# Kernel tuning notes

Hardware: AMD Instinct MI355X
Metric: run time of the kernel (lower is better)

## Reference

```python
import jax, jax.numpy as jnp
import numpy as np


def setup_inputs() -> dict:
    key = jax.random.key(0)
    k1, k2 = jax.random.split(key)
    N, K, D = 32768, 8192, 256
    inputs = jax.random.normal(k1, (N, D), dtype=jnp.float32)
    embedding = jax.random.normal(k2, (K, D), dtype=jnp.float32)  # codebook buffer
    return {"inputs": inputs, "embedding": embedding}


def reference(inputs, embedding):
    # distances[n, k] = ||x_n||^2 + ||e_k||^2 - 2 <x_n, e_k>   (squared L2, as in torch source)
    x_sq = jnp.sum(inputs * inputs, axis=1, keepdims=True)          # [N, 1]
    e_sq = jnp.sum(embedding * embedding, axis=1)                   # [K]
    cross = inputs @ embedding.T                                    # [N, K]
    distances = x_sq + e_sq - 2.0 * cross                           # [N, K]
    encoding_indices = jnp.argmin(distances, axis=1)                # [N] int
    # torch forward returns (None, None, indices); return the tensor output
    return encoding_indices
```

## Files before the change

### kernel.cpp

```cpp
#include <hip/hip_runtime.h>

constexpr int D_DIM   = 256;
constexpr int N_ROWS  = 32768;
constexpr int K_CODES = 8192;
constexpr unsigned TQ = 58;

typedef _Float16 f16x8  __attribute__((ext_vector_type(8)));
typedef __fp16   fp16x2 __attribute__((ext_vector_type(2)));
typedef float    f32x16 __attribute__((ext_vector_type(16)));

#define MFMA32(a, b, c) __builtin_amdgcn_mfma_f32_32x32x16_f16(a, b, c, 0, 0, 0)

__device__ __forceinline__ void cvt_rtn(const float4 a, const float4 b,
                                        uint4& hi, uint4& lo) {
    float f[8] = {a.x, a.y, a.z, a.w, b.x, b.y, b.z, b.w};
    unsigned hb[8], lb[8];
#pragma unroll
    for (int i = 0; i < 8; ++i) {
        _Float16 h = (_Float16)f[i];
        _Float16 l = (_Float16)(f[i] - (float)h);
        hb[i] = __builtin_bit_cast(unsigned short, h);
        lb[i] = __builtin_bit_cast(unsigned short, l);
    }
    hi = make_uint4(hb[0] | (hb[1] << 16), hb[2] | (hb[3] << 16),
                    hb[4] | (hb[5] << 16), hb[6] | (hb[7] << 16));
    lo = make_uint4(lb[0] | (lb[1] << 16), lb[2] | (lb[3] << 16),
                    lb[4] | (lb[5] << 16), lb[6] | (lb[7] << 16));
}

__device__ __forceinline__ void cvt_granule(const float4 a, const float4 b,
                                            uint4& hi, uint4& lo) {
    fp16x2 h0 = __builtin_amdgcn_cvt_pkrtz(a.x, a.y);
    fp16x2 h1 = __builtin_amdgcn_cvt_pkrtz(a.z, a.w);
    fp16x2 h2 = __builtin_amdgcn_cvt_pkrtz(b.x, b.y);
    fp16x2 h3 = __builtin_amdgcn_cvt_pkrtz(b.z, b.w);
    fp16x2 l0 = __builtin_amdgcn_cvt_pkrtz(a.x - (float)h0.x, a.y - (float)h0.y);
    fp16x2 l1 = __builtin_amdgcn_cvt_pkrtz(a.z - (float)h1.x, a.w - (float)h1.y);
    fp16x2 l2 = __builtin_amdgcn_cvt_pkrtz(b.x - (float)h2.x, b.y - (float)h2.y);
    fp16x2 l3 = __builtin_amdgcn_cvt_pkrtz(b.z - (float)h3.x, b.w - (float)h3.y);
    hi = make_uint4(__builtin_bit_cast(unsigned, h0), __builtin_bit_cast(unsigned, h1),
                    __builtin_bit_cast(unsigned, h2), __builtin_bit_cast(unsigned, h3));
    lo = make_uint4(__builtin_bit_cast(unsigned, l0), __builtin_bit_cast(unsigned, l1),
                    __builtin_bit_cast(unsigned, l2), __builtin_bit_cast(unsigned, l3));
}

__device__ __forceinline__ void gl_lds16(const uint4* g, uint4* l) {
    __builtin_amdgcn_global_load_lds(
        (const __attribute__((address_space(1))) void*)g,
        (__attribute__((address_space(3))) void*)l, 16, 0, 0);
}

__global__ __launch_bounds__(256)
void prep_kernel(const float* __restrict__ X, const float* __restrict__ E,
                 uint4* __restrict__ Xh,
                 uint4* __restrict__ Eh, uint4* __restrict__ El,
                 float* __restrict__ esqb, int* __restrict__ cnt) {
    const int tid = threadIdx.x, bid = blockIdx.x;
    if (bid < 1024) {
#pragma unroll 1
        for (int it = 0; it < 4; ++it) {
            const int gid = bid * 1024 + it * 256 + tid;
            const int rb = gid >> 11, rem = gid & 2047;
            const int Lg = rem >> 6, r = rem & 63;
            const float* p = X + (size_t)(rb * 64 + r) * D_DIM + Lg * 8;
            const float4 a = *(const float4*)p, b = *(const float4*)(p + 4);
            uint4 hi, lo; cvt_rtn(a, b, hi, lo);
            Xh[gid] = hi;
        }
    } else if (bid < 1280) {
#pragma unroll 1
        for (int it = 0; it < 4; ++it) {
            const int gid = (bid - 1024) * 1024 + it * 256 + tid;
            const int cb = gid >> 13, rem = gid & 8191;
            const int Lg = rem >> 8, c = rem & 255;
            const float* p = E + (size_t)(cb * 256 + c) * D_DIM + Lg * 8;
            const float4 a = *(const float4*)p, b = *(const float4*)(p + 4);
            uint4 hi, lo; cvt_rtn(a, b, hi, lo);
            Eh[gid] = hi; El[gid] = lo;
        }
    } else {
        if (bid == 1280 && tid == 0) *cnt = 0;
        const int t = (bid - 1280) * 256 + tid;
        const int gw = t >> 6, lane = t & 63;
        const float4 v = ((const float4*)(E + (size_t)gw * D_DIM))[lane];
        float s = v.x * v.x + v.y * v.y + v.z * v.z + v.w * v.w;
#pragma unroll
        for (int off = 32; off; off >>= 1) s += __shfl_down(s, off, 64);
        if (lane == 0) esqb[gw] = s + 1024.0f;
    }
}

__global__ __launch_bounds__(256, 3)
void vq_pass1(const uint4* __restrict__ Xh, const uint4* __restrict__ Eh,
              const float* __restrict__ esqb, uint2* __restrict__ res) {
    __shared__ uint4 sXh[2048];
    __shared__ uint2 slot[4][64];

    const int tid  = threadIdx.x;
    const int lane = tid & 63, wv = tid >> 6;
    const int l31  = lane & 31, lh = lane >> 5;
    const int bid  = blockIdx.x;
    const int bx = bid & 511, strip = bid >> 9;
    const int cs0 = strip * 2048;

    const uint4* Xhb = Xh + bx * 2048;

#pragma unroll
    for (int i = 0; i < 8; ++i)
        gl_lds16(Xhb + i * 256 + tid, &sXh[i * 256 + (wv << 6)]);
    __syncthreads();

    unsigned best[2][16], best2[2][16];
#pragma unroll
    for (int ti = 0; ti < 2; ++ti)
#pragma unroll
        for (int r = 0; r < 16; ++r) { best[ti][r] = 0xFFFFFFFFu; best2[ti][r] = 0xFFFFFFFFu; }

    f32x16 acc[2][2];

#pragma unroll 1
    for (int ct = 0; ct < 8; ++ct) {
        const uint4* __restrict__ Eb =
            Eh + (size_t)(strip * 8 + ct) * 8192 + wv * 64 + l31;

#pragma unroll
        for (int ti = 0; ti < 2; ++ti)
#pragma unroll
            for (int tj = 0; tj < 2; ++tj)
#pragma unroll
                for (int i = 0; i < 16; ++i) acc[ti][tj][i] = 0.0f;

#pragma unroll 4
        for (int k = 0; k < 16; ++k) {
            const int Lg = k * 2 + lh;
            const f16x8 b0 = __builtin_bit_cast(f16x8, Eb[Lg * 256]);
            const f16x8 b1 = __builtin_bit_cast(f16x8, Eb[Lg * 256 + 32]);
            const f16x8 a0 = __builtin_bit_cast(f16x8, sXh[Lg * 64 + l31]);
            const f16x8 a1 = __builtin_bit_cast(f16x8, sXh[Lg * 64 + l31 + 32]);
            acc[0][0] = MFMA32(a0, b0, acc[0][0]);
            acc[0][1] = MFMA32(a0, b1, acc[0][1]);
            acc[1][0] = MFMA32(a1, b0, acc[1][0]);
            acc[1][1] = MFMA32(a1, b1, acc[1][1]);
        }

#pragma unroll
        for (int tj = 0; tj < 2; ++tj) {
            const int code = cs0 + ct * 256 + wv * 64 + tj * 32 + l31;
            const float eb128 = esqb[code] * 128.0f;
#pragma unroll
            for (int ti = 0; ti < 2; ++ti)
#pragma unroll
                for (int r = 0; r < 16; ++r) {
                    const float dq = fmaf(-256.0f, acc[ti][tj][r], eb128);
                    const unsigned q   = (unsigned)dq;
                    const unsigned key = (q << 13) + (unsigned)code;
                    unsigned nb2;
                    asm("v_med3_u32 %0, %1, %2, %3"
                        : "=v"(nb2)
                        : "v"(key), "v"(best[ti][r]), "v"(best2[ti][r]));
                    best2[ti][r] = nb2;
                    best[ti][r]  = key < best[ti][r] ? key : best[ti][r];
                }
        }
    }

#pragma unroll
    for (int ti = 0; ti < 2; ++ti)
#pragma unroll
        for (int r = 0; r < 16; ++r) {
            unsigned b1 = best[ti][r], b2 = best2[ti][r];
#pragma unroll
            for (int m = 16; m >= 1; m >>= 1) {
                const unsigned o1 = (unsigned)__shfl_xor((int)b1, m, 32);
                const unsigned o2 = (unsigned)__shfl_xor((int)b2, m, 32);
                const unsigned t  = b1 > o1 ? b1 : o1;
                b1 = b1 < o1 ? b1 : o1;
                const unsigned m2 = b2 < o2 ? b2 : o2;
                b2 = m2 < t ? m2 : t;
            }
            if (l31 == 0) {
                const int row = ti * 32 + (r & 3) + 8 * (r >> 2) + 4 * lh;
                slot[wv][row] = make_uint2(b1, b2);
            }
        }

    __syncthreads();
    if (tid < 64) {
        const uint2 A = slot[0][tid];
        unsigned b1 = A.x, b2 = A.y;
#pragma unroll
        for (int s = 1; s < 4; ++s) {
            const uint2 B = slot[s][tid];
            const unsigned t  = b1 > B.x ? b1 : B.x;
            b1 = b1 < B.x ? b1 : B.x;
            const unsigned m2 = b2 < B.y ? b2 : B.y;
            b2 = m2 < t ? m2 : t;
        }
        res[(size_t)strip * N_ROWS + bx * 64 + tid] = make_uint2(b1, b2);
    }
}

__global__ void merge_kernel(const uint2* __restrict__ res,
                             unsigned long long* __restrict__ res0,
                             int* __restrict__ out,
                             int* __restrict__ cnt, int* __restrict__ list) {
    const int row = blockIdx.x * 256 + threadIdx.x;
    unsigned b1 = 0xFFFFFFFFu, b2 = 0xFFFFFFFFu;
#pragma unroll
    for (int s = 0; s < 4; ++s) {
        const uint2 v = res[(size_t)s * N_ROWS + row];
        const unsigned t = b1 > v.x ? b1 : v.x;
        b1 = b1 < v.x ? b1 : v.x;
        const unsigned m2 = b2 < v.y ? b2 : v.y;
        b2 = m2 < t ? m2 : t;
    }
    out[row] = (int)(b1 & 8191u);
    if ((b2 >> 13) - (b1 >> 13) < TQ) {
        const int p = atomicAdd(cnt, 1);
        list[p] = row;
        res0[row] = ~0ull;
    }
}

__global__ __launch_bounds__(256, 1)
void refine_kernel(const float* __restrict__ X,
                   const uint4* __restrict__ Eh, const uint4* __restrict__ El,
                   const float* __restrict__ esqb, const int* __restrict__ cnt,
                   const int* __restrict__ list, unsigned long long* __restrict__ res0) {
    __shared__ int  rows_s[32];
    __shared__ uint4 sAh[1024], sAl[1024];

    const int n = *cnt;
    const int base = blockIdx.x * 32;
    if (base >= n) return;
    const int tid = threadIdx.x;
    if (tid < 32) { const int j = base + tid; rows_s[tid] = list[j < n ? j : base]; }
    __syncthreads();

#pragma unroll
    for (int jj = 0; jj < 4; ++jj) {
        const int gg = jj * 256 + tid, Lg = gg >> 5, rr = gg & 31;
        const int row = rows_s[rr];
        const float* p = X + (size_t)row * D_DIM + Lg * 8;
        const float4 a = *(const float4*)p, b = *(const float4*)(p + 4);
        uint4 hi, lo; cvt_rtn(a, b, hi, lo);
        sAh[Lg * 32 + rr] = hi; sAl[Lg * 32 + rr] = lo;
    }
    __syncthreads();

    const int lane = tid & 63, wv = tid >> 6, l31 = lane & 31, lh = lane >> 5;
    const int cbase = blockIdx.y * 1024 + wv * 256;

    float bestv[16]; int besti[16];
#pragma unroll
    for (int r = 0; r < 16; ++r) { bestv[r] = 3.0e38f; besti[r] = 0; }

#pragma unroll 1
    for (int ps = 0; ps < 2; ++ps) {
        const int c0 = cbase + ps * 128;
        f32x16 acc[4];
#pragma unroll
        for (int tj = 0; tj < 4; ++tj)
#pragma unroll
            for (int i = 0; i < 16; ++i) acc[tj][i] = 0.0f;

#pragma unroll
        for (int ks = 0; ks < 16; ++ks) {
            const int Lg = ks * 2 + lh;
            f16x8 b0[4], b1[4];
#pragma unroll
            for (int tj = 0; tj < 4; ++tj) {
                const int c = c0 + tj * 32 + l31;
                const int eg = (c >> 8) * 8192 + Lg * 256 + (c & 255);
                b0[tj] = __builtin_bit_cast(f16x8, Eh[eg]);
                b1[tj] = __builtin_bit_cast(f16x8, El[eg]);
            }
            const f16x8 a0 = __builtin_bit_cast(f16x8, sAh[Lg * 32 + l31]);
            const f16x8 a1 = __builtin_bit_cast(f16x8, sAl[Lg * 32 + l31]);
#pragma unroll
            for (int tj = 0; tj < 4; ++tj) acc[tj] = MFMA32(a1, b0[tj], acc[tj]);
#pragma unroll
            for (int tj = 0; tj < 4; ++tj) acc[tj] = MFMA32(a0, b1[tj], acc[tj]);
#pragma unroll
            for (int tj = 0; tj < 4; ++tj) acc[tj] = MFMA32(a0, b0[tj], acc[tj]);
        }

#pragma unroll
        for (int tj = 0; tj < 4; ++tj) {
            const int c = c0 + tj * 32 + l31;
            const float eb = esqb[c];
#pragma unroll
            for (int r = 0; r < 16; ++r) {
                const float dv = fmaf(-2.0f, acc[tj][r], eb);
                if (dv < bestv[r]) { bestv[r] = dv; besti[r] = c; }
            }
        }
    }

#pragma unroll
    for (int r = 0; r < 16; ++r) {
        float v = bestv[r]; int bi = besti[r];
#pragma unroll
        for (int m = 16; m >= 1; m >>= 1) {
            const float ov = __shfl_xor(v, m, 32);
            const int   oi = __shfl_xor(bi, m, 32);
            if (ov < v || (ov == v && oi < bi)) { v = ov; bi = oi; }
        }
        if (l31 == 0) {
            const int rl = (r & 3) + 8 * (r >> 2) + 4 * lh;
            atomicMin(&res0[rows_s[rl]],
                      ((unsigned long long)__float_as_uint(v) << 32) | (unsigned)bi);
        }
    }
}

__global__ void finalize_kernel(const unsigned long long* __restrict__ res0,
                                const int* __restrict__ cnt, const int* __restrict__ list,
                                int* __restrict__ out) {
    const int i = blockIdx.x * 256 + threadIdx.x;
    if (i < *cnt) {
        const int row = list[i];
        out[row] = (int)(res0[row] & 0xFFFFFFFFull);
    }
}

__global__ void prologue_fb(const float* __restrict__ E, float* __restrict__ esqb,
                            unsigned long long* __restrict__ packed) {
    const int t = blockIdx.x * 256 + threadIdx.x;
    if (t < N_ROWS) packed[t] = ~0ull;
    const int gw = t >> 6, lane = t & 63;
    const float4 v = ((const float4*)(E + (size_t)gw * D_DIM))[lane];
    float s = v.x * v.x + v.y * v.y + v.z * v.z + v.w * v.w;
#pragma unroll
    for (int off = 32; off; off >>= 1) s += __shfl_down(s, off, 64);
    if (lane == 0) esqb[gw] = s + 1024.0f;
}

__global__ __launch_bounds__(256, 2)
void vq_mfma_fallback(const float* __restrict__ X, const float* __restrict__ E,
                      const float* __restrict__ esqb,
                      unsigned long long* __restrict__ packed) {
    __shared__ uint4 fXh[128 * 8], fXl[128 * 8];
    __shared__ uint4 fEh[128 * 8], fEl[128 * 8];
    __shared__ float fEsq[2048];

    const int tid  = threadIdx.x;
    const int lane = tid & 63;
    const int wv   = tid >> 6;
    const int wr   = wv >> 1, wc = wv & 1;
    const int l31  = lane & 31;
    const int lh   = lane >> 5;
    const int row0 = blockIdx.x * 128;
    const int cs0  = blockIdx.y * 2048;

#pragma unroll
    for (int i = 0; i < 8; ++i) fEsq[tid + 256 * i] = esqb[cs0 + tid + 256 * i];

    const int sr = tid >> 3, sg = tid & 7;

    float best[2][16]; int bidx[2][16];
#pragma unroll
    for (int ti = 0; ti < 2; ++ti)
#pragma unroll
        for (int r = 0; r < 16; ++r) { best[ti][r] = 3.0e38f; bidx[ti][r] = 0; }

    f32x16 acc[2][2];

#pragma unroll 1
    for (int ct = 0; ct < 16; ++ct) {
#pragma unroll
        for (int ti = 0; ti < 2; ++ti)
#pragma unroll
            for (int tj = 0; tj < 2; ++tj)
#pragma unroll
                for (int i = 0; i < 16; ++i) acc[ti][tj][i] = 0.0f;

#pragma unroll 1
        for (int dc = 0; dc < 4; ++dc) {
            __syncthreads();
#pragma unroll
            for (int i = 0; i < 4; ++i) {
                const int r = 32 * i + sr;
                const float* p = X + (size_t)(row0 + r) * D_DIM + dc * 64 + sg * 8;
                const float4 a = *(const float4*)p, b = *(const float4*)(p + 4);
                uint4 hi, lo; cvt_granule(a, b, hi, lo);
                const int o = r * 8 + (sg ^ (r & 7));
                fXh[o] = hi; fXl[o] = lo;
            }
#pragma unroll
            for (int i = 0; i < 4; ++i) {
                const int r = 32 * i + sr;
                const float* p = E + (size_t)(cs0 + ct * 128 + r) * D_DIM + dc * 64 + sg * 8;
                const float4 a = *(const float4*)p, b = *(const float4*)(p + 4);
                uint4 hi, lo; cvt_granule(a, b, hi, lo);
                const int o = r * 8 + (sg ^ (r & 7));
                fEh[o] = hi; fEl[o] = lo;
            }
            __syncthreads();

#pragma unroll
            for (int s = 0; s < 4; ++s) {
                const int gi = s * 2 + lh;
                f16x8 axh[2], axl[2], beh[2], bel[2];
#pragma unroll
                for (int ti = 0; ti < 2; ++ti) {
                    const int r = wr * 64 + ti * 32 + l31;
                    const int o = r * 8 + (gi ^ (r & 7));
                    axh[ti] = __builtin_bit_cast(f16x8, fXh[o]);
                    axl[ti] = __builtin_bit_cast(f16x8, fXl[o]);
                }
#pragma unroll
                for (int tj = 0; tj < 2; ++tj) {
                    const int c = wc * 64 + tj * 32 + l31;
                    const int o = c * 8 + (gi ^ (c & 7));
                    beh[tj] = __builtin_bit_cast(f16x8, fEh[o]);
                    bel[tj] = __builtin_bit_cast(f16x8, fEl[o]);
                }
#pragma unroll
                for (int ti = 0; ti < 2; ++ti)
#pragma unroll
                    for (int tj = 0; tj < 2; ++tj) {
                        acc[ti][tj] = MFMA32(axl[ti], beh[tj], acc[ti][tj]);
                        acc[ti][tj] = MFMA32(axh[ti], bel[tj], acc[ti][tj]);
                        acc[ti][tj] = MFMA32(axh[ti], beh[tj], acc[ti][tj]);
                    }
            }
        }

#pragma unroll
        for (int tj = 0; tj < 2; ++tj) {
            const int cloc = ct * 128 + wc * 64 + tj * 32 + l31;
            const float eb = fEsq[cloc];
            const int  code = cs0 + cloc;
#pragma unroll
            for (int ti = 0; ti < 2; ++ti)
#pragma unroll
                for (int r = 0; r < 16; ++r) {
                    const float dv = fmaf(-2.0f, acc[ti][tj][r], eb);
                    if (dv < best[ti][r]) { best[ti][r] = dv; bidx[ti][r] = code; }
                }
        }
    }

#pragma unroll
    for (int ti = 0; ti < 2; ++ti)
#pragma unroll
        for (int r = 0; r < 16; ++r) {
            float b = best[ti][r]; int bi = bidx[ti][r];
#pragma unroll
            for (int m = 16; m >= 1; m >>= 1) {
                const float ov = __shfl_xor(b, m, 32);
                const int   oi = __shfl_xor(bi, m, 32);
                if (ov < b || (ov == b && oi < bi)) { b = ov; bi = oi; }
            }
            if (l31 == 0) {
                const int row = row0 + wr * 64 + ti * 32 + (r & 3) + 8 * (r >> 2) + 4 * lh;
                const unsigned long long p =
                    ((unsigned long long)__float_as_uint(b) << 32) | (unsigned)bi;
                atomicMin(&packed[row], p);
            }
        }
}

__global__ void finish_fb(const unsigned long long* __restrict__ packed,
                          int* __restrict__ out) {
    const int i = blockIdx.x * 256 + threadIdx.x;
    out[i] = (int)(unsigned)(packed[i] & 0xffffffffull);
}

extern "C" void kernel_launch(void* const* d_in, const int* in_sizes, int n_in,
                              void* d_out, int out_size, void* d_ws, size_t ws_size,
                              hipStream_t stream) {
    const float* X = (const float*)d_in[0];
    const float* E = (const float*)d_in[1];
    char* ws = (char*)d_ws;
    int* out = (int*)d_out;

    float* esqb = (float*)ws;
    uint2* res  = (uint2*)(ws + 32768);
    unsigned long long* res0 = (unsigned long long*)(ws + 1081344);
    int* cnt  = (int*)(ws + 1343488);
    int* list = (int*)(ws + 1343504);
    const size_t base = 1572864;
    const size_t szX  = (size_t)N_ROWS * D_DIM * 2;
    const size_t szE  = (size_t)K_CODES * D_DIM * 2;
    const size_t need = base + szX + 2 * szE;

    if (ws_size >= need) {
        uint4* Xh = (uint4*)(ws + base);
        uint4* Eh = (uint4*)(ws + base + szX);
        uint4* El = (uint4*)(ws + base + szX + szE);
        prep_kernel<<<dim3(3328), dim3(256), 0, stream>>>(X, E, Xh, Eh, El, esqb, cnt);
        vq_pass1<<<dim3(2048), dim3(256), 0, stream>>>(Xh, Eh, esqb, res);
        merge_kernel<<<dim3(N_ROWS / 256), dim3(256), 0, stream>>>(res, res0, out, cnt, list);
        refine_kernel<<<dim3(1024, 8), dim3(256), 0, stream>>>(X, Eh, El, esqb,
                                                               cnt, list, res0);
        finalize_kernel<<<dim3(N_ROWS / 256), dim3(256), 0, stream>>>(res0, cnt, list, out);
    } else {
        unsigned long long* packed = (unsigned long long*)(ws + 32768);
        prologue_fb<<<dim3(2048), dim3(256), 0, stream>>>(E, esqb, packed);
        vq_mfma_fallback<<<dim3(N_ROWS / 128, 4), dim3(256), 0, stream>>>(X, E, esqb, packed);
        finish_fb<<<dim3(N_ROWS / 256), dim3(256), 0, stream>>>(packed, out);
    }
}
```

Before: 327.7 us.

## Software-pipeline codebook fragment loads two steps ahead with MFMA priority boost

Adds register double-buffering of the global codebook fragments in vq_pass1: each K step prefetches the B operands two steps ahead, and the first fragments of the next code tile are loaded before the current tile's argmin epilogue. The inner loop is fully unrolled and the MFMA group is wrapped in s_setprio to favour matrix issue. The occupancy hint drops from 3 to 2 waves per SIMD so the extra live registers fit. This aims to hide global load latency behind MFMA work, at the cost of fewer resident waves to cover other stalls.

```diff
diff --git a/kernel.cpp b/kernel.cpp
--- a/kernel.cpp
+++ b/kernel.cpp
@@ -90,7 +90,7 @@
     }
 }
 
-__global__ __launch_bounds__(256, 3)
+__global__ __launch_bounds__(256, 2)
 void vq_pass1(const uint4* __restrict__ Xh, const uint4* __restrict__ Eh,
               const float* __restrict__ esqb, uint2* __restrict__ res) {
     __shared__ uint4 sXh[2048];
@@ -118,11 +118,15 @@
 
     f32x16 acc[2][2];
 
+    const uint4* __restrict__ Eb = Eh + (size_t)(strip * 8) * 8192 + wv * 64 + l31;
+
+    f16x8 pb0 = __builtin_bit_cast(f16x8, Eb[lh * 256]);
+    f16x8 pb1 = __builtin_bit_cast(f16x8, Eb[lh * 256 + 32]);
+    f16x8 pn0 = __builtin_bit_cast(f16x8, Eb[(2 + lh) * 256]);
+    f16x8 pn1 = __builtin_bit_cast(f16x8, Eb[(2 + lh) * 256 + 32]);
+
 #pragma unroll 1
     for (int ct = 0; ct < 8; ++ct) {
-        const uint4* __restrict__ Eb =
-            Eh + (size_t)(strip * 8 + ct) * 8192 + wv * 64 + l31;
-
 #pragma unroll
         for (int ti = 0; ti < 2; ++ti)
 #pragma unroll
@@ -130,17 +134,35 @@
 #pragma unroll
                 for (int i = 0; i < 16; ++i) acc[ti][tj][i] = 0.0f;
 
-#pragma unroll 4
+        f16x8 c0 = pb0, c1 = pb1;
+        f16x8 n0 = pn0, n1 = pn1;
+
+#pragma unroll
         for (int k = 0; k < 16; ++k) {
             const int Lg = k * 2 + lh;
-            const f16x8 b0 = __builtin_bit_cast(f16x8, Eb[Lg * 256]);
-            const f16x8 b1 = __builtin_bit_cast(f16x8, Eb[Lg * 256 + 32]);
+            f16x8 f0, f1;
+            if (k < 14) {
+                f0 = __builtin_bit_cast(f16x8, Eb[(Lg + 4) * 256]);
+                f1 = __builtin_bit_cast(f16x8, Eb[(Lg + 4) * 256 + 32]);
+            }
             const f16x8 a0 = __builtin_bit_cast(f16x8, sXh[Lg * 64 + l31]);
             const f16x8 a1 = __builtin_bit_cast(f16x8, sXh[Lg * 64 + l31 + 32]);
-            acc[0][0] = MFMA32(a0, b0, acc[0][0]);
-            acc[0][1] = MFMA32(a0, b1, acc[0][1]);
-            acc[1][0] = MFMA32(a1, b0, acc[1][0]);
-            acc[1][1] = MFMA32(a1, b1, acc[1][1]);
+            __builtin_amdgcn_s_setprio(1);
+            acc[0][0] = MFMA32(a0, c0, acc[0][0]);
+            acc[0][1] = MFMA32(a0, c1, acc[0][1]);
+            acc[1][0] = MFMA32(a1, c0, acc[1][0]);
+            acc[1][1] = MFMA32(a1, c1, acc[1][1]);
+            __builtin_amdgcn_s_setprio(0);
+            if (k < 15) { c0 = n0; c1 = n1; }
+            if (k < 14) { n0 = f0; n1 = f1; }
+        }
+
+        Eb += 8192;
+        if (ct < 7) {
+            pb0 = __builtin_bit_cast(f16x8, Eb[lh * 256]);
+            pb1 = __builtin_bit_cast(f16x8, Eb[lh * 256 + 32]);
+            pn0 = __builtin_bit_cast(f16x8, Eb[(2 + lh) * 256]);
+            pn1 = __builtin_bit_cast(f16x8, Eb[(2 + lh) * 256 + 32]);
         }
 
 #pragma unroll
```

Result: slower. 402.9 us (+22.9%).

## Software-pipeline MFMA tiles with previous tile's argmin epilogue using double accumulators

Applied to the files above, without the earlier changes.

Restructures the code-tile loop so each tile's MFMA accumulation runs into one accumulator set while the previous tile's distance/argmin epilogue is interleaved in chunks between MFMA groups. It also raises MFMA wave priority with s_setprio. The aim is to hide the VALU-heavy epilogue behind matrix-core work instead of serialising the two. The second accumulator set doubles register pressure, so launch bounds drop from 3 to 2 blocks per SM, which lowers occupancy.

```diff
diff --git a/kernel.cpp b/kernel.cpp
--- a/kernel.cpp
+++ b/kernel.cpp
@@ -90,7 +90,48 @@
     }
 }
 
-__global__ __launch_bounds__(256, 3)
+template<int S, bool EPI>
+__device__ __forceinline__ void kgroup(
+    const uint4* __restrict__ Eb, const uint4 (&sXhp)[2048],
+    const int l31, const int lh,
+    f32x16 (&acc)[2][2], const f32x16 (&accP)[2][2],
+    unsigned (&best)[2][16], unsigned (&best2)[2][16],
+    const float ebp0, const float ebp1, const int codeP) {
+    __builtin_amdgcn_s_setprio(1);
+#pragma unroll
+    for (int j = 0; j < 4; ++j) {
+        const int Lg = (S * 4 + j) * 2 + lh;
+        const f16x8 b0 = __builtin_bit_cast(f16x8, Eb[Lg * 256]);
+        const f16x8 b1 = __builtin_bit_cast(f16x8, Eb[Lg * 256 + 32]);
+        const f16x8 a0 = __builtin_bit_cast(f16x8, sXhp[Lg * 64 + l31]);
+        const f16x8 a1 = __builtin_bit_cast(f16x8, sXhp[Lg * 64 + l31 + 32]);
+        acc[0][0] = MFMA32(a0, b0, acc[0][0]);
+        acc[0][1] = MFMA32(a0, b1, acc[0][1]);
+        acc[1][0] = MFMA32(a1, b0, acc[1][0]);
+        acc[1][1] = MFMA32(a1, b1, acc[1][1]);
+    }
+    __builtin_amdgcn_s_setprio(0);
+    if constexpr (EPI) {
+#pragma unroll
+        for (int u = 0; u < 16; ++u) {
+            const int f  = S * 16 + u;
+            const int tj = f >> 5, ti = (f >> 4) & 1, r = f & 15;
+            const float eb128 = tj ? ebp1 : ebp0;
+            const unsigned code = (unsigned)(codeP + tj * 32);
+            const float dq = fmaf(-256.0f, accP[ti][tj][r], eb128);
+            const unsigned q   = (unsigned)dq;
+            const unsigned key = (q << 13) + code;
+            unsigned nb2;
+            asm("v_med3_u32 %0, %1, %2, %3"
+                : "=v"(nb2)
+                : "v"(key), "v"(best[ti][r]), "v"(best2[ti][r]));
+            best2[ti][r] = nb2;
+            best[ti][r]  = key < best[ti][r] ? key : best[ti][r];
+        }
+    }
+}
+
+__global__ __launch_bounds__(256, 2)
 void vq_pass1(const uint4* __restrict__ Xh, const uint4* __restrict__ Eh,
               const float* __restrict__ esqb, uint2* __restrict__ res) {
     __shared__ uint4 sXh[2048];
@@ -116,44 +157,73 @@
 #pragma unroll
         for (int r = 0; r < 16; ++r) { best[ti][r] = 0xFFFFFFFFu; best2[ti][r] = 0xFFFFFFFFu; }
 
-    f32x16 acc[2][2];
+    f32x16 accA[2][2], accB[2][2];
+
+    auto zacc = [](f32x16 (&a)[2][2]) {
+#pragma unroll
+        for (int ti = 0; ti < 2; ++ti)
+#pragma unroll
+            for (int tj = 0; tj < 2; ++tj)
+#pragma unroll
+                for (int i = 0; i < 16; ++i) a[ti][tj][i] = 0.0f;
+    };
+
+    const uint4* __restrict__ Eb = Eh + (size_t)(strip * 8) * 8192 + wv * 64 + l31;
+    int codeP = cs0 + wv * 64 + l31;
+    float ebP0 = esqb[codeP] * 128.0f;
+    float ebP1 = esqb[codeP + 32] * 128.0f;
+
+    zacc(accA);
+    kgroup<0, false>(Eb, sXh, l31, lh, accA, accA, best, best2, 0.f, 0.f, 0);
+    kgroup<1, false>(Eb, sXh, l31, lh, accA, accA, best, best2, 0.f, 0.f, 0);
+    kgroup<2, false>(Eb, sXh, l31, lh, accA, accA, best, best2, 0.f, 0.f, 0);
+    kgroup<3, false>(Eb, sXh, l31, lh, accA, accA, best, best2, 0.f, 0.f, 0);
 
 #pragma unroll 1
-    for (int ct = 0; ct < 8; ++ct) {
-        const uint4* __restrict__ Eb =
-            Eh + (size_t)(strip * 8 + ct) * 8192 + wv * 64 + l31;
-
-#pragma unroll
-        for (int ti = 0; ti < 2; ++ti)
-#pragma unroll
-            for (int tj = 0; tj < 2; ++tj)
-#pragma unroll
-                for (int i = 0; i < 16; ++i) acc[ti][tj][i] = 0.0f;
-
-#pragma unroll 4
-        for (int k = 0; k < 16; ++k) {
-            const int Lg = k * 2 + lh;
-            const f16x8 b0 = __builtin_bit_cast(f16x8, Eb[Lg * 256]);
-            const f16x8 b1 = __builtin_bit_cast(f16x8, Eb[Lg * 256 + 32]);
-            const f16x8 a0 = __builtin_bit_cast(f16x8, sXh[Lg * 64 + l31]);
-            const f16x8 a1 = __builtin_bit_cast(f16x8, sXh[Lg * 64 + l31 + 32]);
-            acc[0][0] = MFMA32(a0, b0, acc[0][0]);
-            acc[0][1] = MFMA32(a0, b1, acc[0][1]);
-            acc[1][0] = MFMA32(a1, b0, acc[1][0]);
-            acc[1][1] = MFMA32(a1, b1, acc[1][1]);
-        }
+    for (int p = 0; p < 3; ++p) {
+        Eb += 8192;
+        float ebc0 = esqb[codeP + 256] * 128.0f;
+        float ebc1 = esqb[codeP + 288] * 128.0f;
+        zacc(accB);
+        kgroup<0, true>(Eb, sXh, l31, lh, accB, accA, best, best2, ebP0, ebP1, codeP);
+        kgroup<1, true>(Eb, sXh, l31, lh, accB, accA, best, best2, ebP0, ebP1, codeP);
+        kgroup<2, true>(Eb, sXh, l31, lh, accB, accA, best, best2, ebP0, ebP1, codeP);
+        kgroup<3, true>(Eb, sXh, l31, lh, accB, accA, best, best2, ebP0, ebP1, codeP);
+        ebP0 = ebc0; ebP1 = ebc1; codeP += 256;
+
+        Eb += 8192;
+        ebc0 = esqb[codeP + 256] * 128.0f;
+        ebc1 = esqb[codeP + 288] * 128.0f;
+        zacc(accA);
+        kgroup<0, true>(Eb, sXh, l31, lh, accA, accB, best, best2, ebP0, ebP1, codeP);
+        kgroup<1, true>(Eb, sXh, l31, lh, accA, accB, best, best2, ebP0, ebP1, codeP);
+        kgroup<2, true>(Eb, sXh, l31, lh, accA, accB, best, best2, ebP0, ebP1, codeP);
+        kgroup<3, true>(Eb, sXh, l31, lh, accA, accB, best, best2, ebP0, ebP1, codeP);
+        ebP0 = ebc0; ebP1 = ebc1; codeP += 256;
+    }
+
+    Eb += 8192;
+    {
+        const float e70 = esqb[codeP + 256] * 128.0f;
+        const float e71 = esqb[codeP + 288] * 128.0f;
+        zacc(accB);
+        kgroup<0, true>(Eb, sXh, l31, lh, accB, accA, best, best2, ebP0, ebP1, codeP);
+        kgroup<1, true>(Eb, sXh, l31, lh, accB, accA, best, best2, ebP0, ebP1, codeP);
+        kgroup<2, true>(Eb, sXh, l31, lh, accB, accA, best, best2, ebP0, ebP1, codeP);
+        kgroup<3, true>(Eb, sXh, l31, lh, accB, accA, best, best2, ebP0, ebP1, codeP);
+        codeP += 256;
 
 #pragma unroll
         for (int tj = 0; tj < 2; ++tj) {
-            const int code = cs0 + ct * 256 + wv * 64 + tj * 32 + l31;
-            const float eb128 = esqb[code] * 128.0f;
+            const unsigned code = (unsigned)(codeP + tj * 32);
+            const float eb128 = tj ? e71 : e70;
 #pragma unroll
             for (int ti = 0; ti < 2; ++ti)
 #pragma unroll
                 for (int r = 0; r < 16; ++r) {
-                    const float dq = fmaf(-256.0f, acc[ti][tj][r], eb128);
+                    const float dq = fmaf(-256.0f, accB[ti][tj][r], eb128);
                     const unsigned q   = (unsigned)dq;
-                    const unsigned key = (q << 13) + (unsigned)code;
+                    const unsigned key = (q << 13) + code;
                     unsigned nb2;
                     asm("v_med3_u32 %0, %1, %2, %3"
                         : "=v"(nb2)
```

After: 521.4 us. 1.59x slower.
